# Performance work log

Hardware: AMD Instinct MI355X
Metric: run time of the kernel (lower is better)

## Reference

```python
import jax, jax.numpy as jnp
import numpy as np

B, T, C = 2, 2048, 1024
NHEADS = 16
HEAD_DIM = C // NHEADS  # 64
THETA = 10000.0
SCALE_BASE = 512.0
GN_EPS = 1e-5


def setup_inputs() -> dict:
    key = jax.random.key(0)
    ks = jax.random.split(key, 4)
    s = 0.02
    return {
        "x": jax.random.normal(ks[0], (B, T, C), jnp.float32),
        "w_qkv": jax.random.normal(ks[1], (3 * C, C), jnp.float32) * s,
        "w_gated": jax.random.normal(ks[2], (C, C), jnp.float32) * s,
        "w_proj": jax.random.normal(ks[3], (C, C), jnp.float32) * s,
        "gn_weight": jnp.ones((C,), jnp.float32),
        "gn_bias": jnp.zeros((C,), jnp.float32),
    }


def _rotate_half(x):
    # pairs are adjacent/interleaved: (d r) with r=2
    x1 = x[..., 0::2]
    x2 = x[..., 1::2]
    return jnp.stack([-x2, x1], axis=-1).reshape(x.shape)


def _rope_xpos(q, k, T):
    # lucidrains rotary_embedding_torch with use_xpos=True
    d = q.shape[-1]
    half = jnp.arange(0, d, 2, dtype=jnp.float32)
    inv_freq = 1.0 / (THETA ** (half / d))
    t = jnp.arange(T, dtype=jnp.float32)
    freqs = t[:, None] * inv_freq[None, :]          # [T, d/2]
    freqs = jnp.repeat(freqs, 2, axis=-1)           # [T, d] interleaved
    scale_vec = (half + 0.4 * d) / (1.4 * d)        # [d/2]
    power = (t - T // 2) / SCALE_BASE               # [T]
    scale = scale_vec[None, :] ** power[:, None]    # [T, d/2]
    scale = jnp.repeat(scale, 2, axis=-1)           # [T, d]
    cos, sin = jnp.cos(freqs), jnp.sin(freqs)
    q = q * (cos * scale) + _rotate_half(q) * (sin * scale)
    k = k * (cos / scale) + _rotate_half(k) * (sin / scale)
    return q, k


def _decay_mask(T):
    # gamma_h = 1 - 2^(-5-h); mask[h,i,j] = gamma_h^(i-j) for i>=j else 0
    gamma = 1.0 - 2.0 ** (-5.0 - jnp.arange(NHEADS, dtype=jnp.float32))
    idx = jnp.arange(T)
    diff = idx[:, None] - idx[None, :]              # [T, T]
    causal = diff >= 0
    expn = jnp.where(causal, diff, 0).astype(jnp.float32)
    return jnp.where(causal[None], gamma[:, None, None] ** expn[None], 0.0)


def reference(x, w_qkv, w_gated, w_proj, gn_weight, gn_bias):
    Bx, Tx, Cx = x.shape
    qkv = x @ w_qkv.T                               # [B,T,3C]
    q, k, v = jnp.split(qkv, 3, axis=-1)
    def to_heads(u):
        return u.reshape(Bx, Tx, NHEADS, HEAD_DIM).transpose(0, 2, 1, 3)
    q, k, v = to_heads(q), to_heads(k), to_heads(v)  # [B,H,T,D]
    q, k = _rope_xpos(q, k, Tx)
    mask = _decay_mask(Tx)                           # [H,T,T]
    scores = jnp.einsum('bhtd,bhsd->bhts', q, k) * (HEAD_DIM ** -0.5)
    scores = scores * mask[None]
    y = jnp.einsum('bhts,bhsd->bhtd', scores, v)     # [B,H,T,D]
    y = y.transpose(0, 2, 1, 3).reshape(Bx, Tx, Cx)  # [B,T,C]
    # GroupNorm over (B, C, T) with num_groups = NHEADS: normalize each
    # group's (C/H channels x T positions) jointly.
    yt = y.transpose(0, 2, 1).reshape(Bx, NHEADS, HEAD_DIM, Tx)
    mean = yt.mean(axis=(2, 3), keepdims=True)
    var = yt.var(axis=(2, 3), keepdims=True)
    yn = (yt - mean) / jnp.sqrt(var + GN_EPS)
    yn = yn.reshape(Bx, Cx, Tx)
    yn = yn * gn_weight[None, :, None] + gn_bias[None, :, None]
    yn = yn.transpose(0, 2, 1)                       # [B,T,C]
    out = jax.nn.silu(x @ w_gated.T) * yn
    return out @ w_proj.T
```

## Files before the change

kernel.cpp:

```cpp
#include <hip/hip_runtime.h>

typedef __attribute__((ext_vector_type(8))) short bf16x8;
typedef __attribute__((ext_vector_type(4))) float f32x4;
typedef __attribute__((ext_vector_type(16))) float f32x16;
typedef __attribute__((ext_vector_type(2))) unsigned short u16x2;
typedef __attribute__((ext_vector_type(4))) unsigned short u16x4;
typedef __attribute__((ext_vector_type(2))) unsigned int u32x2;

static constexpr int kB = 2;
static constexpr int kT = 2048;
static constexpr int kC = 1024;
static constexpr int kH = 16;
static constexpr int kD = 64;
static constexpr int kNC = 16;

__device__ inline unsigned short f2bf(float f) {
    unsigned int u = __float_as_uint(f);
    u += 0x7FFFu + ((u >> 16) & 1u);
    return (unsigned short)(u >> 16);
}
__device__ inline float bf2f(unsigned short u) {
    return __uint_as_float(((unsigned int)u) << 16);
}

#define GLDS16(g, s)                                                            \
    __builtin_amdgcn_global_load_lds(                                           \
        (const __attribute__((address_space(1))) unsigned int*)(g),             \
        (__attribute__((address_space(3))) unsigned int*)(s), 16, 0, 0)

__global__ __launch_bounds__(256) void cvt_bf16(const float* __restrict__ in,
                                                unsigned short* __restrict__ out, int n) {
    int i = (blockIdx.x * 256 + threadIdx.x) * 4;
    if (i >= n) return;
    float4 v = *(const float4*)(in + i);
    u16x4 o;
    o[0] = f2bf(v.x); o[1] = f2bf(v.y); o[2] = f2bf(v.z); o[3] = f2bf(v.w);
    *(u16x4*)(out + i) = o;
}

__global__ __launch_bounds__(256) void rope_tables(float* __restrict__ ct,
                                                   float* __restrict__ st,
                                                   float* __restrict__ sc) {
    int idx = blockIdx.x * 256 + threadIdx.x;
    if (idx >= kT * 32) return;
    int t = idx >> 5, i = idx & 31;
    float half = 2.0f * (float)i;
    float inv_freq = powf(10000.0f, -half / 64.0f);
    float fr = (float)t * inv_freq;
    float sv = (half + 0.4f * 64.0f) / (1.4f * 64.0f);
    float p = ((float)t - 1024.0f) / 512.0f;
    ct[idx] = cosf(fr);
    st[idx] = sinf(fr);
    sc[idx] = powf(sv, p);
}

__global__ __launch_bounds__(256) void gemm_qkv(const unsigned short* __restrict__ A,
                                                const unsigned short* __restrict__ Bm,
                                                unsigned short* __restrict__ qkb,
                                                unsigned short* __restrict__ vtb) {
    constexpr int K = 1024;
    __shared__ __align__(16) unsigned short Al[128 * 64];
    __shared__ __align__(16) unsigned short Bl[128 * 64];
    char* ab = (char*)Al;
    char* bb = (char*)Bl;
    const int tid = threadIdx.x;
    const int l = tid & 63, w = tid >> 6;
    const int wr = w >> 1, wc = w & 1;
    const int tm = blockIdx.y * 128, tn = blockIdx.x * 128;
    const int ri = l >> 3;
    const int su = (l & 7) ^ (ri & 7);

    f32x4 zero4 = {0.0f, 0.0f, 0.0f, 0.0f};
    f32x4 acc[4][4];
#pragma unroll
    for (int m = 0; m < 4; m++)
#pragma unroll
        for (int n = 0; n < 4; n++) acc[m][n] = zero4;

    for (int kt = 0; kt < K; kt += 64) {
#pragma unroll
        for (int c = w; c < 32; c += 4) {
            if (c < 16) {
                const unsigned short* src = A + (size_t)(tm + c * 8 + ri) * K + kt + su * 8;
                GLDS16(src, ab + c * 1024);
            } else {
                int cb = c - 16;
                const unsigned short* src = Bm + (size_t)(tn + cb * 8 + ri) * K + kt + su * 8;
                GLDS16(src, bb + cb * 1024);
            }
        }
        __syncthreads();
#pragma unroll
        for (int ks = 0; ks < 2; ks++) {
            bf16x8 af[4], bfr[4];
            int kbyte = ks * 64 + (l >> 4) * 16;
#pragma unroll
            for (int m = 0; m < 4; m++) {
                int row = wr * 64 + m * 16 + (l & 15);
                af[m] = *(const bf16x8*)(ab + row * 128 + (kbyte ^ ((row & 7) << 4)));
            }
#pragma unroll
            for (int n = 0; n < 4; n++) {
                int row = wc * 64 + n * 16 + (l & 15);
                bfr[n] = *(const bf16x8*)(bb + row * 128 + (kbyte ^ ((row & 7) << 4)));
            }
#pragma unroll
            for (int m = 0; m < 4; m++)
#pragma unroll
                for (int n = 0; n < 4; n++)
                    acc[m][n] = __builtin_amdgcn_mfma_f32_16x16x32_bf16(af[m], bfr[n], acc[m][n], 0, 0, 0);
        }
        __syncthreads();
    }
    if (tn < 2048) {
#pragma unroll
        for (int m = 0; m < 4; m++)
#pragma unroll
            for (int n = 0; n < 4; n++)
#pragma unroll
                for (int r = 0; r < 4; r++) {
                    int row = tm + wr * 64 + m * 16 + (l >> 4) * 4 + r;
                    int col = tn + wc * 64 + n * 16 + (l & 15);
                    qkb[(size_t)row * 2048 + col] = f2bf(acc[m][n][r]);
                }
    } else {
#pragma unroll
        for (int m = 0; m < 4; m++)
#pragma unroll
            for (int n = 0; n < 4; n++) {
                int col2 = (tn - 2048) + wc * 64 + n * 16 + (l & 15);
                int rowb = tm + wr * 64 + m * 16 + (l >> 4) * 4;
                int b = rowb >> 11, t = rowb & 2047;
                u16x4 o;
#pragma unroll
                for (int r = 0; r < 4; r++) o[r] = f2bf(acc[m][n][r]);
                *(u16x4*)(vtb + ((size_t)(b * 1024 + col2)) * 2048 + t) = o;
            }
    }
}

__global__ __launch_bounds__(256) void rope_qk(const unsigned short* __restrict__ qkb,
                                               const float* __restrict__ ct,
                                               const float* __restrict__ st,
                                               const float* __restrict__ sc,
                                               unsigned short* __restrict__ dq,
                                               unsigned short* __restrict__ dk) {
    int idx = blockIdx.x * 256 + threadIdx.x;
    if (idx >= kB * kT * kH * 32) return;
    int i = idx & 31;
    int h = (idx >> 5) & 15;
    int t = (idx >> 9) & 2047;
    int b = idx >> 20;
    const unsigned short* rowp = qkb + (size_t)(b * kT + t) * 2048 + h * kD + 2 * i;
    u16x2 qv2 = *(const u16x2*)(rowp);
    u16x2 kv2 = *(const u16x2*)(rowp + 1024);
    float qx = bf2f(qv2[0]), qy = bf2f(qv2[1]);
    float kx = bf2f(kv2[0]), ky = bf2f(kv2[1]);
    int ti = t * 32 + i;
    float c = ct[ti], s = st[ti], sv = sc[ti];
    float log2g = log2f(1.0f - exp2f(-5.0f - (float)h));
    float qdec = 0.125f * exp2f(log2g * (float)(t & 127));
    float kdec = exp2f(-log2g * (float)(t & 127));
    float cq = c * sv, sq = s * sv;
    float ck = c / sv, sk = s / sv;
    float q0 = (qx * cq - qy * sq) * qdec;
    float q1 = (qy * cq + qx * sq) * qdec;
    float k0 = (kx * ck - ky * sk) * kdec;
    float k1 = (ky * ck + kx * sk) * kdec;
    size_t doff = (((size_t)(b * kH + h) * kT + t) * kD) + 2 * i;
    u16x2 oq, ok;
    oq[0] = f2bf(q0); oq[1] = f2bf(q1);
    ok[0] = f2bf(k0); ok[1] = f2bf(k1);
    *(u16x2*)(dq + doff) = oq;
    *(u16x2*)(dk + doff) = ok;
}

__global__ __launch_bounds__(256) void kt_bf16(const unsigned short* __restrict__ kb,
                                               unsigned short* __restrict__ ktb) {
    __shared__ unsigned short tile[64][72];
    int tt = blockIdx.x * 64;
    int bh = blockIdx.y;
    int r = threadIdx.x >> 2;
    int cu = (threadIdx.x & 3) * 16;
    const unsigned short* srow = kb + ((size_t)bh * kT + tt + r) * kD + cu;
    bf16x8 i0 = *(const bf16x8*)(srow);
    bf16x8 i1 = *(const bf16x8*)(srow + 8);
#pragma unroll
    for (int e = 0; e < 8; e++) {
        tile[r][cu + e] = (unsigned short)i0[e];
        tile[r][cu + 8 + e] = (unsigned short)i1[e];
    }
    __syncthreads();
    int d = threadIdx.x >> 2;
    int tb = (threadIdx.x & 3) * 16;
    bf16x8 o0, o1;
#pragma unroll
    for (int e = 0; e < 8; e++) {
        o0[e] = (short)tile[tb + e][d];
        o1[e] = (short)tile[tb + 8 + e][d];
    }
    unsigned short* drow = ktb + ((size_t)bh * kD + d) * kT + tt + tb;
    *(bf16x8*)(drow) = o0;
    *(bf16x8*)(drow + 8) = o1;
}

__global__ __launch_bounds__(256) void chunk_m(const unsigned short* __restrict__ ktb,
                                               const unsigned short* __restrict__ vtb,
                                               unsigned short* __restrict__ Mt) {
    __shared__ __align__(16) unsigned short Ktl[64 * 128];
    __shared__ __align__(16) unsigned short Vtl[64 * 128];
    const int tid = threadIdx.x, l = tid & 63, w = tid >> 6;
    const int bh = blockIdx.x, c = blockIdx.y, h = bh & 15;
    const int ql = l & 31, hi5 = l >> 5;
    char* kp = (char*)Ktl;
    char* vp = (char*)Vtl;
#pragma unroll
    for (int j = 0; j < 4; ++j) {
        int ch = w * 4 + j;
        int row = ch * 4 + (l >> 4);
        int u = (l & 15) ^ (row & 15);
        GLDS16(ktb + ((size_t)bh * kD + row) * kT + c * 128 + u * 8, kp + ch * 1024);
        GLDS16(vtb + ((size_t)bh * kD + row) * kT + c * 128 + u * 8, vp + ch * 1024);
    }
    __syncthreads();
    const int iw = w >> 1, jw = w & 1;
    f32x16 acc;
#pragma unroll
    for (int r = 0; r < 16; ++r) acc[r] = 0.0f;
#pragma unroll
    for (int sk = 0; sk < 8; ++sk) {
        int rowa = iw * 32 + ql;
        int rowb = jw * 32 + ql;
        bf16x8 av = *(const bf16x8*)(vp + rowa * 256 + 16 * ((2 * sk + hi5) ^ (rowa & 15)));
        bf16x8 bk = *(const bf16x8*)(kp + rowb * 256 + 16 * ((2 * sk + hi5) ^ (rowb & 15)));
        acc = __builtin_amdgcn_mfma_f32_32x32x16_bf16(av, bk, acc, 0, 0, 0);
    }
    float log2g = log2f(1.0f - exp2f(-5.0f - (float)h));
    float gC = exp2f(128.0f * log2g);
    unsigned short* mo = Mt + ((size_t)(bh * kNC + c)) * 4096;
#pragma unroll
    for (int r = 0; r < 16; ++r) {
        int row = iw * 32 + (r & 3) + 8 * (r >> 2) + 4 * hi5;
        int col = jw * 32 + ql;
        mo[row * 64 + col] = f2bf(acc[r] * gC);
    }
}

__global__ __launch_bounds__(256) void chunk_states(const unsigned short* __restrict__ Mt,
                                                    unsigned short* __restrict__ St) {
    const int bh = blockIdx.x, c = blockIdx.y, h = bh & 15;
    const int tid = threadIdx.x;
    float log2g = log2f(1.0f - exp2f(-5.0f - (float)h));
    float gC = exp2f(128.0f * log2g);
    float acc[16];
#pragma unroll
    for (int e = 0; e < 16; ++e) acc[e] = 0.0f;
    for (int j = 0; j < c; ++j) {
        const unsigned short* m = Mt + ((size_t)(bh * kNC + j)) * 4096;
#pragma unroll
        for (int k = 0; k < 4; ++k) {
            u16x4 v = *(const u16x4*)(m + (k * 256 + tid) * 4);
#pragma unroll
            for (int e = 0; e < 4; ++e) {
                float f = bf2f(v[e]);
                acc[k * 4 + e] = acc[k * 4 + e] * gC + f;
            }
        }
    }
    unsigned short* so = St + ((size_t)(bh * kNC + c)) * 4096;
#pragma unroll
    for (int k = 0; k < 4; ++k) {
        u16x4 o;
#pragma unroll
        for (int e = 0; e < 4; ++e) o[e] = f2bf(acc[k * 4 + e]);
        *(u16x4*)(so + (k * 256 + tid) * 4) = o;
    }
}

__global__ __launch_bounds__(512) void chunk_attn(const unsigned short* __restrict__ qb,
                                                  const unsigned short* __restrict__ kb,
                                                  const unsigned short* __restrict__ vtb,
                                                  const unsigned short* __restrict__ St,
                                                  unsigned short* __restrict__ yb) {
    __shared__ __align__(16) unsigned short Kt[128 * 64];
    __shared__ __align__(16) unsigned short Vt[64 * 128];
    __shared__ __align__(16) unsigned short Ss[64 * 64];
    __shared__ __align__(16) unsigned short Pl[8 * 32 * 64];
    const int tid = threadIdx.x, l = tid & 63, w = tid >> 6;
    const int bh = blockIdx.x, c = blockIdx.y;
    const int qw = w >> 1, dw = w & 1;
    const int ql = l & 31, hi5 = l >> 5;
    char* kp = (char*)Kt;
    char* vp = (char*)Vt;
    char* sp = (char*)Ss;
    char* pw = (char*)Pl + w * 4096;

#pragma unroll
    for (int j = 0; j < 2; ++j) {
        int ch = w * 2 + j;
        int row = ch * 8 + (l >> 3);
        int u = (l & 7) ^ (row & 7);
        GLDS16(kb + ((size_t)bh * kT + c * 128 + row) * kD + u * 8, kp + ch * 1024);
    }
#pragma unroll
    for (int j = 0; j < 2; ++j) {
        int ch = w * 2 + j;
        int row = ch * 4 + (l >> 4);
        int u = (l & 15) ^ (row & 15);
        GLDS16(vtb + ((size_t)bh * kD + row) * kT + c * 128 + u * 8, vp + ch * 1024);
    }
    {
        int row = w * 8 + (l >> 3);
        int u = (l & 7) ^ (row & 7);
        GLDS16(St + ((size_t)(bh * kNC + c)) * 4096 + row * 64 + u * 8, sp + w * 1024);
    }
    bf16x8 aq[4];
    {
        const unsigned short* qrow = qb + ((size_t)bh * kT + c * 128 + qw * 32 + ql) * kD + hi5 * 8;
#pragma unroll
        for (int dk = 0; dk < 4; ++dk) aq[dk] = *(const bf16x8*)(qrow + dk * 16);
    }
    __syncthreads();

    f32x16 acc;
#pragma unroll
    for (int r = 0; r < 16; ++r) acc[r] = 0.0f;
    const int qidx = qw * 32 + ql;

#pragma unroll
    for (int p = 0; p < 2; ++p) {
        f32x16 sA, sB;
#pragma unroll
        for (int r = 0; r < 16; ++r) { sA[r] = 0.0f; sB[r] = 0.0f; }
#pragma unroll
        for (int dk = 0; dk < 4; ++dk) {
            int rowa = (2 * p) * 32 + ql;
            int rowb = (2 * p + 1) * 32 + ql;
            bf16x8 ka = *(const bf16x8*)(kp + rowa * 128 + 16 * ((2 * dk + hi5) ^ (rowa & 7)));
            bf16x8 kb2 = *(const bf16x8*)(kp + rowb * 128 + 16 * ((2 * dk + hi5) ^ (rowb & 7)));
            sA = __builtin_amdgcn_mfma_f32_32x32x16_bf16(ka, aq[dk], sA, 0, 0, 0);
            sB = __builtin_amdgcn_mfma_f32_32x32x16_bf16(kb2, aq[dk], sB, 0, 0, 0);
        }
#pragma unroll
        for (int sb2 = 0; sb2 < 2; ++sb2) {
            int sbase = (2 * p + sb2) * 32 + 4 * hi5;
#pragma unroll
            for (int m = 0; m < 4; ++m) {
                float v0, v1, v2, v3;
                {
                    int s0i = sbase + 8 * m;
                    float x0 = sb2 ? sB[4 * m + 0] : sA[4 * m + 0];
                    float x1 = sb2 ? sB[4 * m + 1] : sA[4 * m + 1];
                    float x2 = sb2 ? sB[4 * m + 2] : sA[4 * m + 2];
                    float x3 = sb2 ? sB[4 * m + 3] : sA[4 * m + 3];
                    v0 = (qidx >= s0i + 0) ? x0 : 0.0f;
                    v1 = (qidx >= s0i + 1) ? x1 : 0.0f;
                    v2 = (qidx >= s0i + 2) ? x2 : 0.0f;
                    v3 = (qidx >= s0i + 3) ? x3 : 0.0f;
                }
                unsigned int lo, hi;
                asm("v_cvt_pk_bf16_f32 %0, %1, %2" : "=v"(lo) : "v"(v0), "v"(v1));
                asm("v_cvt_pk_bf16_f32 %0, %1, %2" : "=v"(hi) : "v"(v2), "v"(v3));
                u32x2 pr; pr[0] = lo; pr[1] = hi;
                *(u32x2*)(pw + ql * 128 + (((sb2 * 4 + m) * 16) ^ ((ql & 7) << 4)) + hi5 * 8) = pr;
            }
        }
#pragma unroll
        for (int kki = 0; kki < 4; ++kki) {
            bf16x8 ap = *(const bf16x8*)(pw + ql * 128 + 16 * ((2 * kki + hi5) ^ (ql & 7)));
            int rowv = dw * 32 + ql;
            bf16x8 bv = *(const bf16x8*)(vp + rowv * 256 + 16 * ((2 * (4 * p + kki) + hi5) ^ (rowv & 15)));
            acc = __builtin_amdgcn_mfma_f32_32x32x16_bf16(ap, bv, acc, 0, 0, 0);
        }
    }
#pragma unroll
    for (int dk = 0; dk < 4; ++dk) {
        int rows = dw * 32 + ql;
        bf16x8 bs = *(const bf16x8*)(sp + rows * 128 + 16 * ((2 * dk + hi5) ^ (rows & 7)));
        acc = __builtin_amdgcn_mfma_f32_32x32x16_bf16(aq[dk], bs, acc, 0, 0, 0);
    }
#pragma unroll
    for (int r = 0; r < 16; ++r) {
        int row = c * 128 + qw * 32 + (r & 3) + 8 * (r >> 2) + 4 * hi5;
        int col = dw * 32 + ql;
        yb[((size_t)bh * kT + row) * kD + col] = f2bf(acc[r]);
    }
}

__global__ __launch_bounds__(256) void gn_part(const unsigned short* __restrict__ yb,
                                               float* __restrict__ part) {
    int bh = blockIdx.y, seg = blockIdx.x;
    const unsigned short* p = yb + (size_t)bh * (kT * kD) + (size_t)seg * (kT * kD / 8);
    float s = 0.0f, s2 = 0.0f;
    for (int i = threadIdx.x; i < (kT * kD / 8) / 8; i += 256) {
        bf16x8 v = *(const bf16x8*)(p + i * 8);
#pragma unroll
        for (int e = 0; e < 8; ++e) {
            float f = bf2f((unsigned short)v[e]);
            s += f; s2 += f * f;
        }
    }
#pragma unroll
    for (int o = 32; o > 0; o >>= 1) {
        s += __shfl_down(s, o);
        s2 += __shfl_down(s2, o);
    }
    __shared__ float red[8];
    int tid = threadIdx.x;
    if ((tid & 63) == 0) {
        red[(tid >> 6) * 2] = s;
        red[(tid >> 6) * 2 + 1] = s2;
    }
    __syncthreads();
    if (tid == 0) {
        float S = 0.0f, S2 = 0.0f;
#pragma unroll
        for (int i = 0; i < 4; i++) { S += red[2 * i]; S2 += red[2 * i + 1]; }
        part[(bh * 8 + seg) * 2] = S;
        part[(bh * 8 + seg) * 2 + 1] = S2;
    }
}

__global__ __launch_bounds__(64) void gn_fin(const float* __restrict__ part,
                                             float* __restrict__ stats) {
    int bh = threadIdx.x;
    if (bh >= kB * kH) return;
    float S = 0.0f, S2 = 0.0f;
#pragma unroll
    for (int i = 0; i < 8; i++) {
        S += part[(bh * 8 + i) * 2];
        S2 += part[(bh * 8 + i) * 2 + 1];
    }
    const float inv = 1.0f / (float)(kT * kD);
    float mean = S * inv;
    float var = S2 * inv - mean * mean;
    stats[2 * bh] = mean;
    stats[2 * bh + 1] = rsqrtf(var + 1e-5f);
}

template <int TN, int EPI>
__global__ __launch_bounds__(256) void gemm_bt(const unsigned short* __restrict__ A,
                                               const unsigned short* __restrict__ Bm,
                                               float* __restrict__ Cf,
                                               unsigned short* __restrict__ Cb,
                                               int N, int K) {
    constexpr int NF = TN / 32;
    constexpr int CH = 16 + TN / 8;
    __shared__ __align__(16) unsigned short Al[128 * 64];
    __shared__ __align__(16) unsigned short Bl[TN * 64];
    char* ab = (char*)Al;
    char* bb = (char*)Bl;
    const int tid = threadIdx.x;
    const int l = tid & 63, w = tid >> 6;
    const int wr = w >> 1, wc = w & 1;
    const int tm = blockIdx.y * 128, tn = blockIdx.x * TN;
    const int ri = l >> 3;
    const int su = (l & 7) ^ (ri & 7);

    f32x4 zero4 = {0.0f, 0.0f, 0.0f, 0.0f};
    f32x4 acc[4][NF];
#pragma unroll
    for (int m = 0; m < 4; m++)
#pragma unroll
        for (int n = 0; n < NF; n++) acc[m][n] = zero4;

    for (int kt = 0; kt < K; kt += 64) {
#pragma unroll
        for (int c = w; c < CH; c += 4) {
            if (c < 16) {
                const unsigned short* src = A + (size_t)(tm + c * 8 + ri) * K + kt + su * 8;
                GLDS16(src, ab + c * 1024);
            } else {
                int cb = c - 16;
                const unsigned short* src = Bm + (size_t)(tn + cb * 8 + ri) * K + kt + su * 8;
                GLDS16(src, bb + cb * 1024);
            }
        }
        __syncthreads();
#pragma unroll
        for (int ks = 0; ks < 2; ks++) {
            bf16x8 af[4], bfr[NF];
            int kbyte = ks * 64 + (l >> 4) * 16;
#pragma unroll
            for (int m = 0; m < 4; m++) {
                int row = wr * 64 + m * 16 + (l & 15);
                af[m] = *(const bf16x8*)(ab + row * 128 + (kbyte ^ ((row & 7) << 4)));
            }
#pragma unroll
            for (int n = 0; n < NF; n++) {
                int row = wc * (TN / 2) + n * 16 + (l & 15);
                bfr[n] = *(const bf16x8*)(bb + row * 128 + (kbyte ^ ((row & 7) << 4)));
            }
#pragma unroll
            for (int m = 0; m < 4; m++)
#pragma unroll
                for (int n = 0; n < NF; n++)
                    acc[m][n] = __builtin_amdgcn_mfma_f32_16x16x32_bf16(af[m], bfr[n], acc[m][n], 0, 0, 0);
        }
        __syncthreads();
    }
#pragma unroll
    for (int m = 0; m < 4; m++)
#pragma unroll
        for (int n = 0; n < NF; n++)
#pragma unroll
            for (int r = 0; r < 4; r++) {
                int row = tm + wr * 64 + m * 16 + (l >> 4) * 4 + r;
                int col = tn + wc * (TN / 2) + n * 16 + (l & 15);
                float v = acc[m][n][r];
                if (EPI == 0) {
                    Cf[(size_t)row * N + col] = v;
                } else {
                    float sv = v / (1.0f + expf(-v));
                    Cb[(size_t)row * N + col] = f2bf(sv);
                }
            }
}

__global__ __launch_bounds__(256) void fuse_z(const unsigned short* __restrict__ gb,
                                              const unsigned short* __restrict__ yb,
                                              const float* __restrict__ stats,
                                              const float* __restrict__ gnw,
                                              const float* __restrict__ gnb,
                                              unsigned short* __restrict__ z) {
    int idx = blockIdx.x * 256 + threadIdx.x;
    int row = idx >> 8;
    int c = (idx & 255) << 2;
    int b = row >> 11, t = row & 2047;
    int h = c >> 6, d = c & 63;
    int bh = b * kH + h;
    u16x4 gv = *(const u16x4*)(gb + (size_t)row * kC + c);
    u16x4 yv = *(const u16x4*)(yb + (((size_t)bh * kT) + t) * kD + d);
    float mean = stats[2 * bh], rstd = stats[2 * bh + 1];
    float4 wv = *(const float4*)(gnw + c);
    float4 bv = *(const float4*)(gnb + c);
    u16x4 o;
    o[0] = f2bf(bf2f(gv[0]) * ((bf2f(yv[0]) - mean) * rstd * wv.x + bv.x));
    o[1] = f2bf(bf2f(gv[1]) * ((bf2f(yv[1]) - mean) * rstd * wv.y + bv.y));
    o[2] = f2bf(bf2f(gv[2]) * ((bf2f(yv[2]) - mean) * rstd * wv.z + bv.z));
    o[3] = f2bf(bf2f(gv[3]) * ((bf2f(yv[3]) - mean) * rstd * wv.w + bv.w));
    *(u16x4*)(z + (size_t)row * kC + c) = o;
}

extern "C" void kernel_launch(void* const* d_in, const int* in_sizes, int n_in,
                              void* d_out, int out_size, void* d_ws, size_t ws_size,
                              hipStream_t stream) {
    const float* x = (const float*)d_in[0];
    const float* w_qkv = (const float*)d_in[1];
    const float* w_gated = (const float*)d_in[2];
    const float* w_proj = (const float*)d_in[3];
    const float* gnw = (const float*)d_in[4];
    const float* gnb = (const float*)d_in[5];
    float* out = (float*)d_out;
    char* ws = (char*)d_ws;

    unsigned short* xb      = (unsigned short*)(ws + 0);
    unsigned short* wqkvb   = (unsigned short*)(ws + 8388608);
    unsigned short* wgatedb = (unsigned short*)(ws + 14680064);
    unsigned short* wprojb  = (unsigned short*)(ws + 16777216);
    unsigned short* qb      = (unsigned short*)(ws + 18874368);
    unsigned short* kbuf    = (unsigned short*)(ws + 27262976);
    unsigned short* vtb     = (unsigned short*)(ws + 35651584);
    unsigned short* zb      = (unsigned short*)(ws + 44040192);
    float* cosT  = (float*)(ws + 52428800);
    float* sinT  = (float*)(ws + 52690944);
    float* sclT  = (float*)(ws + 52953088);
    float* stats = (float*)(ws + 53215232);
    unsigned short* qkb = (unsigned short*)(ws + 53215488);
    unsigned short* ktb = (unsigned short*)(ws + 53215488);
    unsigned short* Mt  = (unsigned short*)(ws + 61604096);
    unsigned short* St  = (unsigned short*)(ws + 65798400);
    unsigned short* yb  = (unsigned short*)(ws + 69992704);
    unsigned short* gbuf= (unsigned short*)(ws + 78381312);
    float* part  = (float*)(ws + 44040192);

    cvt_bf16<<<4096, 256, 0, stream>>>(x, xb, kB * kT * kC);
    cvt_bf16<<<3072, 256, 0, stream>>>(w_qkv, wqkvb, 3 * kC * kC);
    cvt_bf16<<<1024, 256, 0, stream>>>(w_gated, wgatedb, kC * kC);
    cvt_bf16<<<1024, 256, 0, stream>>>(w_proj, wprojb, kC * kC);
    rope_tables<<<256, 256, 0, stream>>>(cosT, sinT, sclT);

    gemm_qkv<<<dim3(3072 / 128, 4096 / 128), 256, 0, stream>>>(xb, wqkvb, qkb, vtb);
    rope_qk<<<8192, 256, 0, stream>>>(qkb, cosT, sinT, sclT, qb, kbuf);

    kt_bf16<<<dim3(kT / 64, kB * kH), 256, 0, stream>>>(kbuf, ktb);

    chunk_m<<<dim3(kB * kH, kNC), 256, 0, stream>>>(ktb, vtb, Mt);
    chunk_states<<<dim3(kB * kH, kNC), 256, 0, stream>>>(Mt, St);
    chunk_attn<<<dim3(kB * kH, kNC), 512, 0, stream>>>(qb, kbuf, vtb, St, yb);

    gn_part<<<dim3(8, kB * kH), 256, 0, stream>>>(yb, part);
    gn_fin<<<1, 64, 0, stream>>>(part, stats);

    gemm_bt<64, 1><<<dim3(kC / 64, 4096 / 128), 256, 0, stream>>>(xb, wgatedb, nullptr, gbuf, kC, kC);
    fuse_z<<<4096, 256, 0, stream>>>(gbuf, yb, stats, gnw, gnb, zb);

    gemm_bt<64, 0><<<dim3(kC / 64, 4096 / 128), 256, 0, stream>>>(zb, wprojb, out, nullptr, kC, kC);
}
```

Before: 147.2 us.

## Fuse RoPE, gated GEMM and GroupNorm stats into neighbouring kernels

The QKV GEMM now also covers the gated projection, since the bf16 w_gated buffer sits directly after w_qkv in the workspace and forms one 4096-row weight matrix. Its epilogue applies RoPE/xPos scaling, the decay and the head-major layout for q/k, and SiLU for the gate, which removes the separate rope_qk kernel, the gated GEMM launch and the intermediate qk buffer round-trip. GroupNorm partial sums are computed in the chunk_attn epilogue instead of a separate gn_part kernel, the output projection uses 128-wide tiles, and a block-index swizzle is added for the big GEMM. The cost is a heavier epilogue, with per-element table loads, a shuffle and scattered 2-byte stores, and more register pressure in the GEMM.

```diff
diff --git a/kernel.cpp b/kernel.cpp
--- a/kernel.cpp
+++ b/kernel.cpp
@@ -54,10 +54,15 @@
     sc[idx] = powf(sv, p);
 }
 
-__global__ __launch_bounds__(256) void gemm_qkv(const unsigned short* __restrict__ A,
-                                                const unsigned short* __restrict__ Bm,
-                                                unsigned short* __restrict__ qkb,
-                                                unsigned short* __restrict__ vtb) {
+__global__ __launch_bounds__(256) void gemm_qkvg(const unsigned short* __restrict__ A,
+                                                 const unsigned short* __restrict__ Bm,
+                                                 const float* __restrict__ ct,
+                                                 const float* __restrict__ st,
+                                                 const float* __restrict__ sc,
+                                                 unsigned short* __restrict__ qb,
+                                                 unsigned short* __restrict__ kbuf,
+                                                 unsigned short* __restrict__ vtb,
+                                                 unsigned short* __restrict__ gbuf) {
     constexpr int K = 1024;
     __shared__ __align__(16) unsigned short Al[128 * 64];
     __shared__ __align__(16) unsigned short Bl[128 * 64];
@@ -66,7 +71,10 @@
     const int tid = threadIdx.x;
     const int l = tid & 63, w = tid >> 6;
     const int wr = w >> 1, wc = w & 1;
-    const int tm = blockIdx.y * 128, tn = blockIdx.x * 128;
+    const int id = blockIdx.x;
+    const int swz = (id & 7) * 128 + (id >> 3);
+    const int by = swz >> 5, bx = swz & 31;
+    const int tm = by * 128, tn = bx * 128;
     const int ri = l >> 3;
     const int su = (l & 7) ^ (ri & 7);
 
@@ -112,18 +120,41 @@
         }
         __syncthreads();
     }
+
     if (tn < 2048) {
-#pragma unroll
-        for (int m = 0; m < 4; m++)
-#pragma unroll
-            for (int n = 0; n < 4; n++)
+        const bool isq = (tn < 1024);
+        unsigned short* dst = isq ? qb : kbuf;
+#pragma unroll
+        for (int n = 0; n < 4; n++) {
+            int col = tn + wc * 64 + n * 16 + (l & 15);
+            int h = (col >> 6) & 15;
+            int d = col & 63;
+            int i = d >> 1;
+            float log2g = log2f(1.0f - exp2f(-5.0f - (float)h));
+#pragma unroll
+            for (int m = 0; m < 4; m++) {
 #pragma unroll
                 for (int r = 0; r < 4; r++) {
                     int row = tm + wr * 64 + m * 16 + (l >> 4) * 4 + r;
-                    int col = tn + wc * 64 + n * 16 + (l & 15);
-                    qkb[(size_t)row * 2048 + col] = f2bf(acc[m][n][r]);
+                    int b = row >> 11, t = row & 2047;
+                    float x = acc[m][n][r];
+                    float xp = __shfl_xor(x, 1);
+                    int ti = t * 32 + i;
+                    float cc = ct[ti], ss = st[ti], sv = sc[ti];
+                    float cs, sn, dec;
+                    if (isq) {
+                        cs = cc * sv; sn = ss * sv;
+                        dec = 0.125f * exp2f(log2g * (float)(t & 127));
+                    } else {
+                        cs = cc / sv; sn = ss / sv;
+                        dec = exp2f(-log2g * (float)(t & 127));
+                    }
+                    float o = ((d & 1) ? (x * cs + xp * sn) : (x * cs - xp * sn)) * dec;
+                    dst[((size_t)(b * 16 + h) * 2048 + t) * 64 + d] = f2bf(o);
                 }
-    } else {
+            }
+        }
+    } else if (tn < 3072) {
 #pragma unroll
         for (int m = 0; m < 4; m++)
 #pragma unroll
@@ -136,43 +167,20 @@
                 for (int r = 0; r < 4; r++) o[r] = f2bf(acc[m][n][r]);
                 *(u16x4*)(vtb + ((size_t)(b * 1024 + col2)) * 2048 + t) = o;
             }
-    }
-}
-
-__global__ __launch_bounds__(256) void rope_qk(const unsigned short* __restrict__ qkb,
-                                               const float* __restrict__ ct,
-                                               const float* __restrict__ st,
-                                               const float* __restrict__ sc,
-                                               unsigned short* __restrict__ dq,
-                                               unsigned short* __restrict__ dk) {
-    int idx = blockIdx.x * 256 + threadIdx.x;
-    if (idx >= kB * kT * kH * 32) return;
-    int i = idx & 31;
-    int h = (idx >> 5) & 15;
-    int t = (idx >> 9) & 2047;
-    int b = idx >> 20;
-    const unsigned short* rowp = qkb + (size_t)(b * kT + t) * 2048 + h * kD + 2 * i;
-    u16x2 qv2 = *(const u16x2*)(rowp);
-    u16x2 kv2 = *(const u16x2*)(rowp + 1024);
-    float qx = bf2f(qv2[0]), qy = bf2f(qv2[1]);
-    float kx = bf2f(kv2[0]), ky = bf2f(kv2[1]);
-    int ti = t * 32 + i;
-    float c = ct[ti], s = st[ti], sv = sc[ti];
-    float log2g = log2f(1.0f - exp2f(-5.0f - (float)h));
-    float qdec = 0.125f * exp2f(log2g * (float)(t & 127));
-    float kdec = exp2f(-log2g * (float)(t & 127));
-    float cq = c * sv, sq = s * sv;
-    float ck = c / sv, sk = s / sv;
-    float q0 = (qx * cq - qy * sq) * qdec;
-    float q1 = (qy * cq + qx * sq) * qdec;
-    float k0 = (kx * ck - ky * sk) * kdec;
-    float k1 = (ky * ck + kx * sk) * kdec;
-    size_t doff = (((size_t)(b * kH + h) * kT + t) * kD) + 2 * i;
-    u16x2 oq, ok;
-    oq[0] = f2bf(q0); oq[1] = f2bf(q1);
-    ok[0] = f2bf(k0); ok[1] = f2bf(k1);
-    *(u16x2*)(dq + doff) = oq;
-    *(u16x2*)(dk + doff) = ok;
+    } else {
+#pragma unroll
+        for (int m = 0; m < 4; m++)
+#pragma unroll
+            for (int n = 0; n < 4; n++)
+#pragma unroll
+                for (int r = 0; r < 4; r++) {
+                    int row = tm + wr * 64 + m * 16 + (l >> 4) * 4 + r;
+                    int col3 = (tn - 3072) + wc * 64 + n * 16 + (l & 15);
+                    float v = acc[m][n][r];
+                    float sv2 = v / (1.0f + expf(-v));
+                    gbuf[(size_t)row * 1024 + col3] = f2bf(sv2);
+                }
+    }
 }
 
 __global__ __launch_bounds__(256) void kt_bf16(const unsigned short* __restrict__ kb,
@@ -281,11 +289,13 @@
                                                   const unsigned short* __restrict__ kb,
                                                   const unsigned short* __restrict__ vtb,
                                                   const unsigned short* __restrict__ St,
-                                                  unsigned short* __restrict__ yb) {
+                                                  unsigned short* __restrict__ yb,
+                                                  float* __restrict__ part) {
     __shared__ __align__(16) unsigned short Kt[128 * 64];
     __shared__ __align__(16) unsigned short Vt[64 * 128];
     __shared__ __align__(16) unsigned short Ss[64 * 64];
     __shared__ __align__(16) unsigned short Pl[8 * 32 * 64];
+    __shared__ float red[16];
     const int tid = threadIdx.x, l = tid & 63, w = tid >> 6;
     const int bh = blockIdx.x, c = blockIdx.y;
     const int qw = w >> 1, dw = w & 1;
@@ -379,45 +389,29 @@
         bf16x8 bs = *(const bf16x8*)(sp + rows * 128 + 16 * ((2 * dk + hi5) ^ (rows & 7)));
         acc = __builtin_amdgcn_mfma_f32_32x32x16_bf16(aq[dk], bs, acc, 0, 0, 0);
     }
+    float s = 0.0f, s2 = 0.0f;
 #pragma unroll
     for (int r = 0; r < 16; ++r) {
         int row = c * 128 + qw * 32 + (r & 3) + 8 * (r >> 2) + 4 * hi5;
         int col = dw * 32 + ql;
-        yb[((size_t)bh * kT + row) * kD + col] = f2bf(acc[r]);
-    }
-}
-
-__global__ __launch_bounds__(256) void gn_part(const unsigned short* __restrict__ yb,
-                                               float* __restrict__ part) {
-    int bh = blockIdx.y, seg = blockIdx.x;
-    const unsigned short* p = yb + (size_t)bh * (kT * kD) + (size_t)seg * (kT * kD / 8);
-    float s = 0.0f, s2 = 0.0f;
-    for (int i = threadIdx.x; i < (kT * kD / 8) / 8; i += 256) {
-        bf16x8 v = *(const bf16x8*)(p + i * 8);
-#pragma unroll
-        for (int e = 0; e < 8; ++e) {
-            float f = bf2f((unsigned short)v[e]);
-            s += f; s2 += f * f;
-        }
+        unsigned short ub = f2bf(acc[r]);
+        yb[((size_t)bh * kT + row) * kD + col] = ub;
+        float f = bf2f(ub);
+        s += f; s2 += f * f;
     }
 #pragma unroll
     for (int o = 32; o > 0; o >>= 1) {
         s += __shfl_down(s, o);
         s2 += __shfl_down(s2, o);
     }
-    __shared__ float red[8];
-    int tid = threadIdx.x;
-    if ((tid & 63) == 0) {
-        red[(tid >> 6) * 2] = s;
-        red[(tid >> 6) * 2 + 1] = s2;
-    }
+    if (l == 0) { red[w * 2] = s; red[w * 2 + 1] = s2; }
     __syncthreads();
     if (tid == 0) {
         float S = 0.0f, S2 = 0.0f;
 #pragma unroll
-        for (int i = 0; i < 4; i++) { S += red[2 * i]; S2 += red[2 * i + 1]; }
-        part[(bh * 8 + seg) * 2] = S;
-        part[(bh * 8 + seg) * 2 + 1] = S2;
+        for (int i = 0; i < 8; i++) { S += red[2 * i]; S2 += red[2 * i + 1]; }
+        part[((size_t)bh * kNC + c) * 2] = S;
+        part[((size_t)bh * kNC + c) * 2 + 1] = S2;
     }
 }
 
@@ -427,9 +421,9 @@
     if (bh >= kB * kH) return;
     float S = 0.0f, S2 = 0.0f;
 #pragma unroll
-    for (int i = 0; i < 8; i++) {
-        S += part[(bh * 8 + i) * 2];
-        S2 += part[(bh * 8 + i) * 2 + 1];
+    for (int i = 0; i < kNC; i++) {
+        S += part[(bh * kNC + i) * 2];
+        S2 += part[(bh * kNC + i) * 2 + 1];
     }
     const float inv = 1.0f / (float)(kT * kD);
     float mean = S * inv;
@@ -438,35 +432,31 @@
     stats[2 * bh + 1] = rsqrtf(var + 1e-5f);
 }
 
-template <int TN, int EPI>
-__global__ __launch_bounds__(256) void gemm_bt(const unsigned short* __restrict__ A,
-                                               const unsigned short* __restrict__ Bm,
-                                               float* __restrict__ Cf,
-                                               unsigned short* __restrict__ Cb,
-                                               int N, int K) {
-    constexpr int NF = TN / 32;
-    constexpr int CH = 16 + TN / 8;
+__global__ __launch_bounds__(256) void gemm_proj(const unsigned short* __restrict__ A,
+                                                 const unsigned short* __restrict__ Bm,
+                                                 float* __restrict__ Cf,
+                                                 int N, int K) {
     __shared__ __align__(16) unsigned short Al[128 * 64];
-    __shared__ __align__(16) unsigned short Bl[TN * 64];
+    __shared__ __align__(16) unsigned short Bl[128 * 64];
     char* ab = (char*)Al;
     char* bb = (char*)Bl;
     const int tid = threadIdx.x;
     const int l = tid & 63, w = tid >> 6;
     const int wr = w >> 1, wc = w & 1;
-    const int tm = blockIdx.y * 128, tn = blockIdx.x * TN;
+    const int tm = blockIdx.y * 128, tn = blockIdx.x * 128;
     const int ri = l >> 3;
     const int su = (l & 7) ^ (ri & 7);
 
     f32x4 zero4 = {0.0f, 0.0f, 0.0f, 0.0f};
-    f32x4 acc[4][NF];
+    f32x4 acc[4][4];
 #pragma unroll
     for (int m = 0; m < 4; m++)
 #pragma unroll
-        for (int n = 0; n < NF; n++) acc[m][n] = zero4;
+        for (int n = 0; n < 4; n++) acc[m][n] = zero4;
 
     for (int kt = 0; kt < K; kt += 64) {
 #pragma unroll
-        for (int c = w; c < CH; c += 4) {
+        for (int c = w; c < 32; c += 4) {
             if (c < 16) {
                 const unsigned short* src = A + (size_t)(tm + c * 8 + ri) * K + kt + su * 8;
                 GLDS16(src, ab + c * 1024);
@@ -479,7 +469,7 @@
         __syncthreads();
 #pragma unroll
         for (int ks = 0; ks < 2; ks++) {
-            bf16x8 af[4], bfr[NF];
+            bf16x8 af[4], bfr[4];
             int kbyte = ks * 64 + (l >> 4) * 16;
 #pragma unroll
             for (int m = 0; m < 4; m++) {
@@ -487,14 +477,14 @@
                 af[m] = *(const bf16x8*)(ab + row * 128 + (kbyte ^ ((row & 7) << 4)));
             }
 #pragma unroll
-            for (int n = 0; n < NF; n++) {
-                int row = wc * (TN / 2) + n * 16 + (l & 15);
+            for (int n = 0; n < 4; n++) {
+                int row = wc * 64 + n * 16 + (l & 15);
                 bfr[n] = *(const bf16x8*)(bb + row * 128 + (kbyte ^ ((row & 7) << 4)));
             }
 #pragma unroll
             for (int m = 0; m < 4; m++)
 #pragma unroll
-                for (int n = 0; n < NF; n++)
+                for (int n = 0; n < 4; n++)
                     acc[m][n] = __builtin_amdgcn_mfma_f32_16x16x32_bf16(af[m], bfr[n], acc[m][n], 0, 0, 0);
         }
         __syncthreads();
@@ -502,18 +492,12 @@
 #pragma unroll
     for (int m = 0; m < 4; m++)
 #pragma unroll
-        for (int n = 0; n < NF; n++)
+        for (int n = 0; n < 4; n++)
 #pragma unroll
             for (int r = 0; r < 4; r++) {
                 int row = tm + wr * 64 + m * 16 + (l >> 4) * 4 + r;
-                int col = tn + wc * (TN / 2) + n * 16 + (l & 15);
-                float v = acc[m][n][r];
-                if (EPI == 0) {
-                    Cf[(size_t)row * N + col] = v;
-                } else {
-                    float sv = v / (1.0f + expf(-v));
-                    Cb[(size_t)row * N + col] = f2bf(sv);
-                }
+                int col = tn + wc * 64 + n * 16 + (l & 15);
+                Cf[(size_t)row * N + col] = acc[m][n][r];
             }
 }
 
@@ -566,12 +550,11 @@
     float* sinT  = (float*)(ws + 52690944);
     float* sclT  = (float*)(ws + 52953088);
     float* stats = (float*)(ws + 53215232);
-    unsigned short* qkb = (unsigned short*)(ws + 53215488);
-    unsigned short* ktb = (unsigned short*)(ws + 53215488);
-    unsigned short* Mt  = (unsigned short*)(ws + 61604096);
-    unsigned short* St  = (unsigned short*)(ws + 65798400);
-    unsigned short* yb  = (unsigned short*)(ws + 69992704);
-    unsigned short* gbuf= (unsigned short*)(ws + 78381312);
+    unsigned short* Mt  = (unsigned short*)(ws + 53215488);
+    unsigned short* St  = (unsigned short*)(ws + 57409792);
+    unsigned short* yb  = (unsigned short*)(ws + 61604096);
+    unsigned short* gbuf= (unsigned short*)(ws + 69992704);
+    unsigned short* ktb = (unsigned short*)(ws + 78381312);
     float* part  = (float*)(ws + 44040192);
 
     cvt_bf16<<<4096, 256, 0, stream>>>(x, xb, kB * kT * kC);
@@ -580,20 +563,17 @@
     cvt_bf16<<<1024, 256, 0, stream>>>(w_proj, wprojb, kC * kC);
     rope_tables<<<256, 256, 0, stream>>>(cosT, sinT, sclT);
 
-    gemm_qkv<<<dim3(3072 / 128, 4096 / 128), 256, 0, stream>>>(xb, wqkvb, qkb, vtb);
-    rope_qk<<<8192, 256, 0, stream>>>(qkb, cosT, sinT, sclT, qb, kbuf);
+    gemm_qkvg<<<1024, 256, 0, stream>>>(xb, wqkvb, cosT, sinT, sclT, qb, kbuf, vtb, gbuf);
 
     kt_bf16<<<dim3(kT / 64, kB * kH), 256, 0, stream>>>(kbuf, ktb);
 
     chunk_m<<<dim3(kB * kH, kNC), 256, 0, stream>>>(ktb, vtb, Mt);
     chunk_states<<<dim3(kB * kH, kNC), 256, 0, stream>>>(Mt, St);
-    chunk_attn<<<dim3(kB * kH, kNC), 512, 0, stream>>>(qb, kbuf, vtb, St, yb);
-
-    gn_part<<<dim3(8, kB * kH), 256, 0, stream>>>(yb, part);
+    chunk_attn<<<dim3(kB * kH, kNC), 512, 0, stream>>>(qb, kbuf, vtb, St, yb, part);
+
     gn_fin<<<1, 64, 0, stream>>>(part, stats);
 
-    gemm_bt<64, 1><<<dim3(kC / 64, 4096 / 128), 256, 0, stream>>>(xb, wgatedb, nullptr, gbuf, kC, kC);
     fuse_z<<<4096, 256, 0, stream>>>(gbuf, yb, stats, gnw, gnb, zb);
 
-    gemm_bt<64, 0><<<dim3(kC / 64, 4096 / 128), 256, 0, stream>>>(zb, wprojb, out, nullptr, kC, kC);
-}
+    gemm_proj<<<dim3(kC / 128, 4096 / 128), 256, 0, stream>>>(zb, wprojb, out, kC, kC);
+}
```

Measured after the change: 143.3 us. 1.03x faster.
